# Kernel optimization log

Measured on AMD Instinct MI355X. Metric: run time of the kernel, lower is better.

The kernel has to match this reference:

```python
import jax, jax.numpy as jnp
import numpy as np

CM = 8        # channel_mult
EPS = 1e-5    # BatchNorm eps
NEG = 0.2     # LeakyReLU slope


def conv2d(x, w, stride, pad, b=None):
    y = jax.lax.conv_general_dilated(
        x, w, (stride, stride), [(pad, pad), (pad, pad)],
        dimension_numbers=('NCHW', 'OIHW', 'NCHW'))
    if b is not None:
        y = y + b[None, :, None, None]
    return y


def per_sample_conv(x, w, stride, pad):
    # x: [B,C,H,W], w: [B,O,C,kh,kw] -> per-sample conv, vmapped over batch
    f = lambda xi, wi: conv2d(xi[None], wi, stride, pad)[0]
    return jax.vmap(f)(x, w)


def batchnorm(x, g, b):
    # training-mode BN: batch statistics over (N,H,W)
    m = jnp.mean(x, axis=(0, 2, 3), keepdims=True)
    v = jnp.var(x, axis=(0, 2, 3), keepdims=True)
    return (x - m) * jax.lax.rsqrt(v + EPS) * g[None, :, None, None] + b[None, :, None, None]


def lrelu(x):
    return jnp.where(x >= 0, x, NEG * x)


def setup_inputs() -> dict:
    key = jax.random.key(0)
    ks = jax.random.split(key, 16)
    B, H, W = 16, 512, 512

    def rn(k, shape, fan_in):
        return jax.random.normal(k, shape, jnp.float32) * np.float32(1.0 / np.sqrt(fan_in))

    inp = {}
    inp['x'] = jax.random.normal(ks[0], (B, 3, H, W), jnp.float32)
    n_meta = 3 * (CM // 2) * 25 + CM * (CM * 2 // 2) * 25  # 300 + 1600 = 1900
    inp['conv_weights'] = jax.random.normal(ks[1], (B, n_meta), jnp.float32) * 0.05
    inp['w11'] = rn(ks[2], (CM // 2, 3, 5, 5), 3 * 25)
    inp['b11'] = jnp.zeros((CM // 2,), jnp.float32)
    inp['w12'] = rn(ks[3], (CM * 2 // 2, CM, 5, 5), CM * 25)
    inp['b12'] = jnp.zeros((CM * 2 // 2,), jnp.float32)
    inp['bn1_g'] = jnp.ones((CM * 2,), jnp.float32)
    inp['bn1_b'] = jnp.zeros((CM * 2,), jnp.float32)
    # conv2 stack: (in, out, kernel)
    chans = [(CM * 2, CM * 4, 5), (CM * 4, CM * 8, 5), (CM * 8, CM * 16, 3), (CM * 16, CM * 16, 3)]
    for i, (ci, co, k) in enumerate(chans, 1):
        inp[f'c2w{i}'] = rn(ks[3 + i], (co, ci, k, k), ci * k * k)
        inp[f'c2b{i}'] = jnp.zeros((co,), jnp.float32)
        inp[f'bn{i}g'] = jnp.ones((co,), jnp.float32)
        inp[f'bn{i}b'] = jnp.zeros((co,), jnp.float32)
    return inp


def reference(x, conv_weights, w11, b11, w12, b12, bn1_g, bn1_b,
              c2w1, c2b1, bn1g, bn1b, c2w2, c2b2, bn2g, bn2b,
              c2w3, c2b3, bn3g, bn3b, c2w4, c2b4, bn4g, bn4b):
    B, _, H, W = x.shape
    n1 = 3 * (CM // 2) * 25
    w1 = conv_weights[:, :n1].reshape(B, CM // 2, 3, 5, 5)
    w2 = conv_weights[:, n1:].reshape(B, CM * 2 // 2, CM, 5, 5)

    # meta layer 1: shared half + per-sample dynamic half
    xx = conv2d(x, w11, 1, 2, b11)                  # [B, cm/2, H, W]
    half = per_sample_conv(x, w1, 1, 2)             # [B, cm/2, H, W]
    h = lrelu(jnp.concatenate([xx, half], axis=1))  # [B, cm, H, W]

    # meta layer 2 (stride 2)
    xx = conv2d(h, w12, 2, 2, b12)                  # [B, cm, H/2, W/2]
    half = per_sample_conv(h, w2, 2, 2)             # [B, cm, H/2, W/2]
    h = lrelu(batchnorm(jnp.concatenate([xx, half], axis=1), bn1_g, bn1_b))

    # dense conv stack
    for w_, b_, g_, be_, p in [
        (c2w1, c2b1, bn1g, bn1b, 2),
        (c2w2, c2b2, bn2g, bn2b, 2),
        (c2w3, c2b3, bn3g, bn3b, 1),
        (c2w4, c2b4, bn4g, bn4b, 1),
    ]:
        h = lrelu(batchnorm(conv2d(h, w_, 2, p, b_), g_, be_))

    return h.reshape(-1, CM * 16, H // 32, W // 32)
```

## Files before the change

kernel.cpp:

```cpp
#include <hip/hip_runtime.h>


typedef __attribute__((ext_vector_type(8))) short short8v;
typedef __attribute__((ext_vector_type(4))) float float4v;
typedef unsigned short u16;

#define LRELU_NEG 0.2f
#define BN_EPS 1e-5f

__device__ __forceinline__ float bf2f(u16 u){ union{unsigned i; float f;} v; v.i=(unsigned)u<<16; return v.f; }
__device__ __forceinline__ u16 f2bf(float f){ unsigned x=__float_as_uint(f); x += 0x7FFFu + ((x>>16)&1u); return (u16)(x>>16); }
__device__ __forceinline__ float lrelu(float v){ return v<0.f? LRELU_NEG*v : v; }

__device__ __forceinline__ void packw(int i, const float* __restrict__ w, u16* __restrict__ dst,
                                      int IC, int OC, int KSZ, int CPR) {
  int kq = i & 31, oc = (i>>5) % OC, c = i/(OC*32);
  int ky = c / CPR, r = c % CPR;
  int kk = r*32 + kq; int kx = kk / IC, ic = kk % IC;
  float v = (kx < KSZ) ? w[(((size_t)oc*IC + ic)*KSZ + ky)*KSZ + kx] : 0.f;
  dst[i] = f2bf(v);
}

__global__ __launch_bounds__(256) void prep_all(
    const float* __restrict__ w11, const float* __restrict__ w12,
    const float* __restrict__ b12, const float* __restrict__ cw,
    const float* __restrict__ wc1, const float* __restrict__ wc2,
    const float* __restrict__ wc3, const float* __restrict__ wc4,
    u16* __restrict__ wl1m, u16* __restrict__ wl2m, float* __restrict__ bl2,
    u16* __restrict__ d1, u16* __restrict__ d2, u16* __restrict__ d3, u16* __restrict__ d4,
    u16* __restrict__ h1) {
  int i = blockIdx.x*256 + threadIdx.x;
  if (i < 16) {
    bl2[i] = (i<8)? b12[i] : 0.f;
  } else if (i < 40976) {
    int j = i - 16;
    int b = j / 2560, r = j % 2560;
    int ky = r >> 9, r2 = r & 511;
    int oc = r2 >> 5, kk = r2 & 31;
    int kx = kk >> 2, ic = kk & 3;
    float v = 0.f;
    if (ic < 3 && kx < 5 && oc < 8)
      v = (oc < 4) ? w11[((oc*3+ic)*5+ky)*5+kx]
                   : cw[b*1900 + (oc-4)*75 + ic*25 + ky*5 + kx];
    wl1m[j] = f2bf(v);
  } else if (i < 122896) {
    int j = i - 40976;
    int kq = j & 31, oc = (j>>5) & 15, c = (j>>9) % 10, b = j / 5120;
    int ky = c >> 1, r = c & 1;
    int kk = r*32 + kq; int kx = kk >> 3, ic = kk & 7;
    float v = 0.f;
    if (kx < 5)
      v = (oc < 8) ? w12[((oc*8+ic)*5+ky)*5+kx]
                   : cw[b*1900 + 300 + ((oc-8)*8+ic)*25 + ky*5 + kx];
    wl2m[j] = f2bf(v);
  } else if (i < 188688) {
    int j = i - 122896;
    int b = j / 4112, p = j % 4112;
    int y, xx;
    if (p < 2064) { int r = p/516; y = (r<2)? r : 512+r; xx = p%516; }
    else          { int q = p-2064; int cidx = q&3; xx = (cidx<2)? cidx : 512+cidx; y = 2 + (q>>2); }
    short8v z = {0,0,0,0,0,0,0,0};
    *(short8v*)(h1 + (((size_t)b*516 + y)*516 + xx)*8) = z;
  } else if (i < 476432) {
    int j = i - 188688;
    if (j < 15360) packw(j, wc1, d1, 16, 32, 5, 3);
    else if (j < 66560) packw(j-15360, wc2, d2, 32, 64, 5, 5);
    else if (j < 140288) packw(j-66560, wc3, d3, 64, 128, 3, 6);
    else packw(j-140288, wc4, d4, 128, 128, 3, 12);
  }
}

__global__ __launch_bounds__(256) void conv_l1(const float* __restrict__ x,
    const u16* __restrict__ wl1m, const float* __restrict__ b11,
    u16* __restrict__ h1) {
  __shared__ u16 sx[12*72*4];
  const int tid = threadIdx.x, b = blockIdx.z;
  const int x0 = (blockIdx.x & 7) * 64;
  const int r0 = (blockIdx.x >> 3) * 8;

  for (int e = tid; e < 864; e += 256) {
    int row = e / 72, col = e % 72;
    int gy = r0 + row - 2, gx = x0 + col - 2;
    float v0 = 0.f, v1 = 0.f, v2 = 0.f;
    if (gy >= 0 && gy < 512 && gx >= 0 && gx < 512) {
      size_t base = ((size_t)b*3*512 + gy)*512 + gx;
      v0 = x[base]; v1 = x[base + 262144]; v2 = x[base + 524288];
    }
    ushort4 pk = {f2bf(v0), f2bf(v1), f2bf(v2), 0};
    *(ushort4*)(sx + e*4) = pk;
  }
  __syncthreads();

  const int lane = tid & 63, w = tid >> 6;
  const int l15 = lane & 15, sub = lane >> 4;

  short8v Bf[5];
  const u16* wb = wl1m + (size_t)b*2560;
#pragma unroll
  for (int c = 0; c < 5; c++)
    Bf[c] = *(const short8v*)(wb + (c*16 + l15)*32 + sub*8);
  const float bv = (l15 < 4) ? b11[l15] : 0.f;

  const int colb = w*16 + l15;
#pragma unroll 2
  for (int ly = 0; ly < 8; ly++) {
    float4v acc = {0.f, 0.f, 0.f, 0.f};
#pragma unroll
    for (int c = 0; c < 5; c++) {
      const u16* ap = sx + (((ly + c)*72 + colb) << 2) + sub*8;
      union { unsigned long long q[2]; short8v v; } ua;
      ua.q[0] = *(const unsigned long long*)(ap);
      ua.q[1] = *(const unsigned long long*)(ap + 4);
      acc = __builtin_amdgcn_mfma_f32_16x16x32_bf16(ua.v, Bf[c], acc, 0, 0, 0);
    }
    if (l15 < 8) {
      size_t rb = (((size_t)b*516 + r0 + ly + 2)*516 + x0 + w*16 + sub*4 + 2)*8 + l15;
#pragma unroll
      for (int r = 0; r < 4; r++)
        h1[rb + r*8] = f2bf(lrelu(acc[r] + bv));
    }
  }
}

template <int IC, int OC, int KSZ, int S, int P, int CPR, int NCH,
          int IPH, int IPW, int OWL, int OPH, int OPW,
          int WM, int WN, int WVM, int WVN, bool PERS>
__global__ __launch_bounds__(WVM*WVN*64) void conv_mfma(
    const u16* __restrict__ in, const u16* __restrict__ wmfma,
    const float* __restrict__ bias, u16* __restrict__ out,
    float2* __restrict__ part2) {
  constexpr int OW = 1 << OWL;
  constexpr int PADOFF = 2 - P;
  const int tid = threadIdx.x, lane = tid & 63;
  const int w = tid >> 6, wm = w % WVM, wn = w / WVM;
  const int l15 = lane & 15, sub = lane >> 4;
  const int b = blockIdx.z;
  const int px0 = blockIdx.x * (16*WM*WVM) + wm * (16*WM);
  const int oc0 = blockIdx.y * (16*WN*WVN) + wn * (16*WN);

  int oyf[WM], oxb[WM], ixb[WM];
#pragma unroll
  for (int f = 0; f < WM; f++) {
    int p = px0 + f*16;
    oyf[f] = p >> OWL;
    oxb[f] = p & (OW-1);
    ixb[f] = S*(oxb[f] + l15) + PADOFF;
  }
  const u16* inb = in + (size_t)b*IPH*IPW*IC;
  const u16* wbase = wmfma + (PERS ? (size_t)b*NCH*OC*32 : (size_t)0);

  float4v acc[WM][WN];
#pragma unroll
  for (int f = 0; f < WM; f++)
#pragma unroll
    for (int n = 0; n < WN; n++) acc[f][n] = (float4v){0.f,0.f,0.f,0.f};

#pragma unroll
  for (int ky = 0; ky < KSZ; ky++) {
#pragma unroll
    for (int r = 0; r < CPR; r++) {
      const int c = ky*CPR + r;
      const int kk0 = r*32 + sub*8;
      const int kx = kk0 / IC;
      const int icoff = kk0 % IC;
      short8v B[WN];
#pragma unroll
      for (int n = 0; n < WN; n++)
        B[n] = *(const short8v*)(wbase + ((size_t)c*OC + oc0 + n*16 + l15)*32 + sub*8);
      short8v A[WM];
#pragma unroll
      for (int f = 0; f < WM; f++) {
        int iy = S*oyf[f] + ky + PADOFF;
        A[f] = *(const short8v*)(inb + ((size_t)iy*IPW + ixb[f] + kx)*IC + icoff);
      }
#pragma unroll
      for (int f = 0; f < WM; f++)
#pragma unroll
        for (int n = 0; n < WN; n++)
          acc[f][n] = __builtin_amdgcn_mfma_f32_16x16x32_bf16(A[f], B[n], acc[f][n], 0, 0, 0);
    }
  }

  float s[WN], q[WN];
#pragma unroll
  for (int n = 0; n < WN; n++) { s[n] = 0.f; q[n] = 0.f; }
#pragma unroll
  for (int f = 0; f < WM; f++) {
    const int oxs = oxb[f] + sub*4;
    const size_t rowb = ((size_t)b*OPH + oyf[f] + 2)*OPW;
#pragma unroll
    for (int n = 0; n < WN; n++) {
      int oc = oc0 + n*16 + l15;
      float bv = bias[oc];
#pragma unroll
      for (int rr = 0; rr < 4; rr++) {
        float v = acc[f][n][rr] + bv;
        out[(rowb + oxs + rr + 2)*OC + oc] = f2bf(v);
        s[n] += v; q[n] += v*v;
      }
    }
  }
#pragma unroll
  for (int n = 0; n < WN; n++) {
    s[n] += __shfl_xor(s[n], 16); s[n] += __shfl_xor(s[n], 32);
    q[n] += __shfl_xor(q[n], 16); q[n] += __shfl_xor(q[n], 32);
  }
  __shared__ float sred[WVM*WVN][WN][16][2];
  if (sub == 0) {
#pragma unroll
    for (int n = 0; n < WN; n++) { sred[w][n][l15][0] = s[n]; sred[w][n][l15][1] = q[n]; }
  }
  __syncthreads();
  const int NBp = gridDim.x * gridDim.z;
  const int pb = blockIdx.z * gridDim.x + blockIdx.x;
  const int tot = WVN*WN*16;
  if (tid < tot) {
    int c16 = tid & 15, n = (tid >> 4) % WN, wn2 = tid / (16*WN);
    float S_ = 0.f, Q_ = 0.f;
    for (int wm2 = 0; wm2 < WVM; wm2++) {
      S_ += sred[wn2*WVM + wm2][n][c16][0];
      Q_ += sred[wn2*WVM + wm2][n][c16][1];
    }
    int c = blockIdx.y*(16*WN*WVN) + wn2*(16*WN) + n*16 + c16;
    part2[(size_t)c*NBp + pb] = make_float2(S_, Q_);
  }
}

__global__ void bn_stage2(const float2* __restrict__ part2, const float* __restrict__ g,
                          const float* __restrict__ bb, float* __restrict__ stats,
                          int NBp, float invN) {
  int c = blockIdx.x;
  float s = 0.f, q = 0.f;
  for (int i = threadIdx.x; i < NBp; i += 64) {
    float2 p = part2[(size_t)c*NBp + i];
    s += p.x; q += p.y;
  }
  for (int o = 32; o > 0; o >>= 1) { s += __shfl_down(s, o); q += __shfl_down(q, o); }
  if (threadIdx.x == 0) {
    float m = s * invN;
    float var = q * invN - m*m;
    float sc = g[c] * rsqrtf(var + BN_EPS);
    stats[2*c] = sc;
    stats[2*c+1] = bb[c] - m*sc;
  }
}

template <int C, int PH, int PW, int HH, int WW>
__global__ __launch_bounds__(256) void bn_fin(u16* __restrict__ y, const float* __restrict__ stats,
                                              int total8) {
  int i = blockIdx.x*256 + threadIdx.x;
  if (i >= total8) return;
  size_t e = (size_t)i*8;
  int c0 = (int)(e & (C-1));
  int px = (int)(e / C);
  int xx = px % PW;
  int yy = (px / PW) % PH;
  bool interior = (yy >= 2) & (yy < 2+HH) & (xx >= 2) & (xx < 2+WW);
  short8v u = *(short8v*)(y + e);
  short8v o;
#pragma unroll
  for (int j = 0; j < 8; j++) {
    float v = bf2f((u16)u[j]) * stats[2*(c0+j)] + stats[2*(c0+j)+1];
    o[j] = interior ? (short)f2bf(lrelu(v)) : (short)0;
  }
  *(short8v*)(y + e) = o;
}

__global__ __launch_bounds__(256) void out_k(const u16* __restrict__ y6,
                                             const float* __restrict__ stats,
                                             float* __restrict__ out) {
  int i = blockIdx.x*256 + threadIdx.x;
  if (i >= 131072) return;
  size_t e = (size_t)i*4;
  int c0 = (int)(e & 127);
  int px = (int)(e >> 7);
  int loc = px & 255, b = px >> 8;
  int y = loc >> 4, x = loc & 15;
  const u16* src = y6 + (((size_t)b*20 + y + 2)*20 + x + 2)*128 + c0;
  ushort4 u = *(const ushort4*)src;
  float vv[4] = {bf2f(u.x), bf2f(u.y), bf2f(u.z), bf2f(u.w)};
#pragma unroll
  for (int j = 0; j < 4; j++) {
    int c = c0 + j;
    float v = vv[j] * stats[2*c] + stats[2*c+1];
    out[(((size_t)b*128 + c) << 8) + loc] = lrelu(v);
  }
}

extern "C" void kernel_launch(void* const* d_in, const int* in_sizes, int n_in,
                              void* d_out, int out_size, void* d_ws, size_t ws_size,
                              hipStream_t stream) {
  const float* x    = (const float*)d_in[0];
  const float* cw   = (const float*)d_in[1];
  const float* w11  = (const float*)d_in[2];
  const float* b11  = (const float*)d_in[3];
  const float* w12  = (const float*)d_in[4];
  const float* b12  = (const float*)d_in[5];
  const float* bn1g = (const float*)d_in[6];
  const float* bn1b = (const float*)d_in[7];
  const float* c2w[4] = {(const float*)d_in[8], (const float*)d_in[12],
                         (const float*)d_in[16], (const float*)d_in[20]};
  const float* c2b[4] = {(const float*)d_in[9], (const float*)d_in[13],
                         (const float*)d_in[17], (const float*)d_in[21]};
  const float* bng[4] = {(const float*)d_in[10], (const float*)d_in[14],
                         (const float*)d_in[18], (const float*)d_in[22]};
  const float* bnb[4] = {(const float*)d_in[11], (const float*)d_in[15],
                         (const float*)d_in[19], (const float*)d_in[23]};

  char* ws = (char*)d_ws;
  u16* h1   = (u16*)(ws);
  u16* y3   = (u16*)(ws);
  u16* y4   = (u16*)(ws + 17842176);
  u16* y5   = (u16*)(ws + 27312128);
  u16* y6   = (u16*)(ws + 32620544);
  u16* yT2  = (u16*)(ws + 68158464);
  u16* wl2m = (u16*)(ws + 102769664);
  float* bl2    = (float*)(ws + 102933504);
  float2* part2 = (float2*)(ws + 102933568);
  float* stats2 = (float*)(ws + 103457856);
  float* stats3 = stats2 + 32;
  float* stats4 = stats3 + 64;
  float* stats5 = stats4 + 128;
  float* stats6 = stats5 + 256;
  u16* wl1m = (u16*)(ws + 103460800);
  u16* wS1  = (u16*)(ws + 103542720);
  u16* wS2  = (u16*)(ws + 103573440);
  u16* wS3  = (u16*)(ws + 103675840);
  u16* wS4  = (u16*)(ws + 103823296);

  prep_all<<<1862, 256, 0, stream>>>(w11, w12, b12, cw,
                                     c2w[0], c2w[1], c2w[2], c2w[3],
                                     wl1m, wl2m, bl2, wS1, wS2, wS3, wS4, h1);

  conv_l1<<<dim3(512, 1, 16), 256, 0, stream>>>(x, wl1m, b11, h1);

  conv_mfma<8,16,5,2,2, 2,10, 516,516, 8, 260,260, 4,1,4,1, true>
      <<<dim3(256,1,16), 256, 0, stream>>>(h1, wl2m, bl2, yT2, part2);

  bn_stage2<<<16, 64, 0, stream>>>(part2, bn1g, bn1b, stats2, 4096, 1.f/1048576.f);
  bn_fin<16,260,260,256,256><<<8450, 256, 0, stream>>>(yT2, stats2, 2163200);

  conv_mfma<16,32,5,2,2, 3,15, 260,260, 7, 132,132, 2,2,4,1, false>
      <<<dim3(128,1,16), 256, 0, stream>>>(yT2, wS1, c2b[0], y3, part2);
  bn_stage2<<<32, 64, 0, stream>>>(part2, bng[0], bnb[0], stats3, 2048, 1.f/262144.f);
  bn_fin<32,132,132,128,128><<<4356, 256, 0, stream>>>(y3, stats3, 1115136);

  conv_mfma<32,64,5,2,2, 5,25, 132,132, 6, 68,68, 2,2,2,2, false>
      <<<dim3(64,1,16), 256, 0, stream>>>(y3, wS2, c2b[1], y4, part2);
  bn_stage2<<<64, 64, 0, stream>>>(part2, bng[1], bnb[1], stats4, 1024, 1.f/65536.f);
  bn_fin<64,68,68,64,64><<<2312, 256, 0, stream>>>(y4, stats4, 591872);

  conv_mfma<64,128,3,2,1, 6,18, 68,68, 5, 36,36, 2,2,2,2, false>
      <<<dim3(16,2,16), 256, 0, stream>>>(y4, wS3, c2b[2], y5, part2);
  bn_stage2<<<128, 64, 0, stream>>>(part2, bng[2], bnb[2], stats5, 256, 1.f/16384.f);
  bn_fin<128,36,36,32,32><<<1296, 256, 0, stream>>>(y5, stats5, 331776);

  conv_mfma<128,128,3,2,1, 12,36, 36,36, 4, 20,20, 2,2,1,2, false>
      <<<dim3(8,2,16), 128, 0, stream>>>(y5, wS4, c2b[3], y6, part2);
  bn_stage2<<<128, 64, 0, stream>>>(part2, bng[3], bnb[3], stats6, 128, 1.f/4096.f);

  out_k<<<512, 256, 0, stream>>>(y6, stats6, (float*)d_out);
}
```

Before: 277.2 us.

## Compute two output rows per MFMA in layer-1 conv with row-shifted weights

Layer-1 weights are repacked so that each 16-wide MFMA operand holds two output rows times eight channels, using shifted ky offsets across six row chunks. Each wave now issues 4×6 MFMAs instead of 8×5 and writes four channels per lane as one vectorized store, rather than eight scalar stores from only half the lanes. Interior tiles also skip bounds checks when loading the input halo. The cost is a larger, zero-padded weight buffer and shifted workspace offsets.

```diff
diff --git a/kernel.cpp b/kernel.cpp
--- a/kernel.cpp
+++ b/kernel.cpp
@@ -3,6 +3,7 @@
 
 typedef __attribute__((ext_vector_type(8))) short short8v;
 typedef __attribute__((ext_vector_type(4))) float float4v;
+typedef __attribute__((ext_vector_type(4))) unsigned short ushort4v;
 typedef unsigned short u16;
 
 #define LRELU_NEG 0.2f
@@ -26,25 +27,27 @@
     const float* __restrict__ b12, const float* __restrict__ cw,
     const float* __restrict__ wc1, const float* __restrict__ wc2,
     const float* __restrict__ wc3, const float* __restrict__ wc4,
-    u16* __restrict__ wl1m, u16* __restrict__ wl2m, float* __restrict__ bl2,
+    u16* __restrict__ wl1d, u16* __restrict__ wl2m, float* __restrict__ bl2,
     u16* __restrict__ d1, u16* __restrict__ d2, u16* __restrict__ d3, u16* __restrict__ d4,
     u16* __restrict__ h1) {
   int i = blockIdx.x*256 + threadIdx.x;
   if (i < 16) {
     bl2[i] = (i<8)? b12[i] : 0.f;
-  } else if (i < 40976) {
+  } else if (i < 49168) {
     int j = i - 16;
-    int b = j / 2560, r = j % 2560;
-    int ky = r >> 9, r2 = r & 511;
-    int oc = r2 >> 5, kk = r2 & 31;
+    int b = j / 3072, r = j % 3072;
+    int c = r >> 9, r2 = r & 511;
+    int row = r2 >> 5, kk = r2 & 31;
     int kx = kk >> 2, ic = kk & 3;
+    int grp = row >> 3, oc = row & 7;
+    int ky = c - grp;
     float v = 0.f;
-    if (ic < 3 && kx < 5 && oc < 8)
+    if (ic < 3 && kx < 5 && ky >= 0 && ky < 5)
       v = (oc < 4) ? w11[((oc*3+ic)*5+ky)*5+kx]
                    : cw[b*1900 + (oc-4)*75 + ic*25 + ky*5 + kx];
-    wl1m[j] = f2bf(v);
-  } else if (i < 122896) {
-    int j = i - 40976;
+    wl1d[j] = f2bf(v);
+  } else if (i < 131088) {
+    int j = i - 49168;
     int kq = j & 31, oc = (j>>5) & 15, c = (j>>9) % 10, b = j / 5120;
     int ky = c >> 1, r = c & 1;
     int kk = r*32 + kq; int kx = kk >> 3, ic = kk & 7;
@@ -53,16 +56,16 @@
       v = (oc < 8) ? w12[((oc*8+ic)*5+ky)*5+kx]
                    : cw[b*1900 + 300 + ((oc-8)*8+ic)*25 + ky*5 + kx];
     wl2m[j] = f2bf(v);
-  } else if (i < 188688) {
-    int j = i - 122896;
+  } else if (i < 196880) {
+    int j = i - 131088;
     int b = j / 4112, p = j % 4112;
     int y, xx;
     if (p < 2064) { int r = p/516; y = (r<2)? r : 512+r; xx = p%516; }
     else          { int q = p-2064; int cidx = q&3; xx = (cidx<2)? cidx : 512+cidx; y = 2 + (q>>2); }
     short8v z = {0,0,0,0,0,0,0,0};
     *(short8v*)(h1 + (((size_t)b*516 + y)*516 + xx)*8) = z;
-  } else if (i < 476432) {
-    int j = i - 188688;
+  } else if (i < 484624) {
+    int j = i - 196880;
     if (j < 15360) packw(j, wc1, d1, 16, 32, 5, 3);
     else if (j < 66560) packw(j-15360, wc2, d2, 32, 64, 5, 5);
     else if (j < 140288) packw(j-66560, wc3, d3, 64, 128, 3, 6);
@@ -71,54 +74,70 @@
 }
 
 __global__ __launch_bounds__(256) void conv_l1(const float* __restrict__ x,
-    const u16* __restrict__ wl1m, const float* __restrict__ b11,
+    const u16* __restrict__ wl1d, const float* __restrict__ b11,
     u16* __restrict__ h1) {
   __shared__ u16 sx[12*72*4];
   const int tid = threadIdx.x, b = blockIdx.z;
   const int x0 = (blockIdx.x & 7) * 64;
   const int r0 = (blockIdx.x >> 3) * 8;
 
-  for (int e = tid; e < 864; e += 256) {
-    int row = e / 72, col = e % 72;
-    int gy = r0 + row - 2, gx = x0 + col - 2;
-    float v0 = 0.f, v1 = 0.f, v2 = 0.f;
-    if (gy >= 0 && gy < 512 && gx >= 0 && gx < 512) {
-      size_t base = ((size_t)b*3*512 + gy)*512 + gx;
-      v0 = x[base]; v1 = x[base + 262144]; v2 = x[base + 524288];
-    }
-    ushort4 pk = {f2bf(v0), f2bf(v1), f2bf(v2), 0};
-    *(ushort4*)(sx + e*4) = pk;
+  const bool interior = (r0 >= 2) & (r0 <= 502) & (x0 >= 2) & (x0 <= 442);
+  if (interior) {
+    for (int e = tid; e < 864; e += 256) {
+      int row = e / 72, col = e % 72;
+      size_t base = ((size_t)b*3*512 + r0 + row - 2)*512 + x0 + col - 2;
+      ushort4 pk = {f2bf(x[base]), f2bf(x[base + 262144]), f2bf(x[base + 524288]), 0};
+      *(ushort4*)(sx + e*4) = pk;
+    }
+  } else {
+    for (int e = tid; e < 864; e += 256) {
+      int row = e / 72, col = e % 72;
+      int gy = r0 + row - 2, gx = x0 + col - 2;
+      float v0 = 0.f, v1 = 0.f, v2 = 0.f;
+      if (gy >= 0 && gy < 512 && gx >= 0 && gx < 512) {
+        size_t base = ((size_t)b*3*512 + gy)*512 + gx;
+        v0 = x[base]; v1 = x[base + 262144]; v2 = x[base + 524288];
+      }
+      ushort4 pk = {f2bf(v0), f2bf(v1), f2bf(v2), 0};
+      *(ushort4*)(sx + e*4) = pk;
+    }
   }
   __syncthreads();
 
   const int lane = tid & 63, w = tid >> 6;
   const int l15 = lane & 15, sub = lane >> 4;
 
-  short8v Bf[5];
-  const u16* wb = wl1m + (size_t)b*2560;
-#pragma unroll
-  for (int c = 0; c < 5; c++)
-    Bf[c] = *(const short8v*)(wb + (c*16 + l15)*32 + sub*8);
-  const float bv = (l15 < 4) ? b11[l15] : 0.f;
+  short8v Wf[6];
+  const u16* wb = wl1d + (size_t)b*3072;
+#pragma unroll
+  for (int c = 0; c < 6; c++)
+    Wf[c] = *(const short8v*)(wb + (c*16 + l15)*32 + sub*8);
+
+  float bvv[4];
+#pragma unroll
+  for (int r = 0; r < 4; r++) bvv[r] = (sub & 1) ? 0.f : b11[r];
 
   const int colb = w*16 + l15;
-#pragma unroll 2
-  for (int ly = 0; ly < 8; ly++) {
+  const int oc0 = (sub & 1) * 4;
+  const int rsel = sub >> 1;
+
+#pragma unroll
+  for (int p = 0; p < 4; p++) {
     float4v acc = {0.f, 0.f, 0.f, 0.f};
 #pragma unroll
-    for (int c = 0; c < 5; c++) {
-      const u16* ap = sx + (((ly + c)*72 + colb) << 2) + sub*8;
+    for (int c = 0; c < 6; c++) {
+      const u16* ap = sx + (((2*p + c)*72 + colb) << 2) + sub*8;
       union { unsigned long long q[2]; short8v v; } ua;
       ua.q[0] = *(const unsigned long long*)(ap);
       ua.q[1] = *(const unsigned long long*)(ap + 4);
-      acc = __builtin_amdgcn_mfma_f32_16x16x32_bf16(ua.v, Bf[c], acc, 0, 0, 0);
-    }
-    if (l15 < 8) {
-      size_t rb = (((size_t)b*516 + r0 + ly + 2)*516 + x0 + w*16 + sub*4 + 2)*8 + l15;
-#pragma unroll
-      for (int r = 0; r < 4; r++)
-        h1[rb + r*8] = f2bf(lrelu(acc[r] + bv));
-    }
+      acc = __builtin_amdgcn_mfma_f32_16x16x32_bf16(Wf[c], ua.v, acc, 0, 0, 0);
+    }
+    ushort4v pk;
+#pragma unroll
+    for (int r = 0; r < 4; r++) pk[r] = f2bf(lrelu(acc[r] + bvv[r]));
+    int outrow = r0 + 2*p + rsel;
+    u16* dst = h1 + (((size_t)b*516 + outrow + 2)*516 + x0 + colb + 2)*8 + oc0;
+    *(ushort4v*)dst = pk;
   }
 }
 
@@ -322,17 +341,17 @@
   float* stats4 = stats3 + 64;
   float* stats5 = stats4 + 128;
   float* stats6 = stats5 + 256;
-  u16* wl1m = (u16*)(ws + 103460800);
-  u16* wS1  = (u16*)(ws + 103542720);
-  u16* wS2  = (u16*)(ws + 103573440);
-  u16* wS3  = (u16*)(ws + 103675840);
-  u16* wS4  = (u16*)(ws + 103823296);
-
-  prep_all<<<1862, 256, 0, stream>>>(w11, w12, b12, cw,
+  u16* wl1d = (u16*)(ws + 103460800);
+  u16* wS1  = (u16*)(ws + 103559104);
+  u16* wS2  = (u16*)(ws + 103589824);
+  u16* wS3  = (u16*)(ws + 103692224);
+  u16* wS4  = (u16*)(ws + 103839680);
+
+  prep_all<<<1894, 256, 0, stream>>>(w11, w12, b12, cw,
                                      c2w[0], c2w[1], c2w[2], c2w[3],
-                                     wl1m, wl2m, bl2, wS1, wS2, wS3, wS4, h1);
-
-  conv_l1<<<dim3(512, 1, 16), 256, 0, stream>>>(x, wl1m, b11, h1);
+                                     wl1d, wl2m, bl2, wS1, wS2, wS3, wS4, h1);
+
+  conv_l1<<<dim3(512, 1, 16), 256, 0, stream>>>(x, wl1d, b11, h1);
 
   conv_mfma<8,16,5,2,2, 2,10, 516,516, 8, 260,260, 4,1,4,1, true>
       <<<dim3(256,1,16), 256, 0, stream>>>(h1, wl2m, bl2, yT2, part2);
```

Result: faster. 271.7 us (-2.0%).
